# Performance work log

Hardware: AMD Instinct MI355X
Metric: run time of the kernel (lower is better)

The kernel has to match this reference:

```python
import math
import jax, jax.numpy as jnp
import numpy as np

B, T, S = 4, 4096, 1024
HID, CTX, EMB, H = 1024, 768, 1024, 16
D = EMB // H  # head_dim = 64


def setup_inputs() -> dict:
    key = jax.random.key(0)
    ks = jax.random.split(key, 7)
    sc = lambda n: 1.0 / math.sqrt(n)
    return {
        "tokens": jax.random.normal(ks[0], (B, T, HID), jnp.float32),
        "context": jax.random.normal(ks[1], (B, S, CTX), jnp.float32),
        "Wq": jax.random.normal(ks[2], (HID, EMB), jnp.float32) * sc(HID),
        "Wk": jax.random.normal(ks[3], (CTX, EMB), jnp.float32) * sc(CTX),
        "Wv": jax.random.normal(ks[4], (CTX, EMB), jnp.float32) * sc(CTX),
        "Wo": jax.random.normal(ks[5], (EMB, HID), jnp.float32) * sc(EMB),
        "bo": jnp.zeros((HID,), jnp.float32),
    }


def reference(tokens, context, Wq, Wk, Wv, Wo, bo):
    # projections (bias-free, as in torch Linear(bias=False))
    Q = tokens @ Wq              # [B,T,EMB]
    K = context @ Wk             # [B,S,EMB]
    V = context @ Wv             # [B,S,EMB]
    # split heads: B T (H D) -> B H T D
    Q = Q.reshape(B, T, H, D).transpose(0, 2, 1, 3)
    K = K.reshape(B, S, H, D).transpose(0, 2, 1, 3)
    V = V.reshape(B, S, H, D).transpose(0, 2, 1, 3)
    scores = jnp.einsum('bhtd,bhsd->bhts', Q, K) / math.sqrt(D)
    attn = jax.nn.softmax(scores, axis=-1)
    ctx = jnp.einsum('bhts,bhsd->bhtd', attn, V)
    ctx = ctx.transpose(0, 2, 1, 3).reshape(B, T, EMB)
    return ctx @ Wo + bo
```

## Files before the change

kernel.cpp:

```cpp
#include <hip/hip_runtime.h>
#include <hip/hip_bf16.h>

#define B_ 4
#define T_ 4096
#define S_ 1024
#define HID_ 1024
#define CTX_ 768
#define EMB_ 1024
#define H_ 16
#define D_ 64

#define QSCALE 0.18033688011112042f

typedef __attribute__((ext_vector_type(8))) short short8;
typedef __attribute__((ext_vector_type(4))) float f32x4;
typedef __attribute__((ext_vector_type(4))) unsigned short us4;
typedef unsigned short ushort_t;

__device__ inline ushort_t f2b(float f) {
  union { float f; unsigned u; } x; x.f = f;
  return (ushort_t)((x.u + 0x7fffu + ((x.u >> 16) & 1u)) >> 16);
}
__device__ inline unsigned cvtpk2(float a, float b) {
  __hip_bfloat162 h = __float22bfloat162_rn(float2{a, b});
  union { __hip_bfloat162 h; unsigned u; } c; c.h = h; return c.u;
}
__device__ inline ushort_t f2b_fast(float f) {
  __hip_bfloat16 h = __float2bfloat16(f);
  union { __hip_bfloat16 h; ushort_t u; } c; c.h = h; return c.u;
}

using gu32p = const __attribute__((address_space(1))) unsigned int*;
using lu32p = __attribute__((address_space(3))) unsigned int*;
__device__ inline void gload16(const ushort_t* g, ushort_t* l) {
  __builtin_amdgcn_global_load_lds((gu32p)(const void*)g, (lu32p)(void*)l, 16, 0, 0);
}

__device__ inline void conv_body(const float* __restrict__ in, ushort_t* __restrict__ out,
                                 int blk, int tid) {
  const size_t i = ((size_t)blk * 256 + tid) * 8;
  const float4 a = *(const float4*)(in + i);
  const float4 b = *(const float4*)(in + i + 4);
  uint4 u;
  u.x = cvtpk2(a.x, a.y); u.y = cvtpk2(a.z, a.w);
  u.z = cvtpk2(b.x, b.y); u.w = cvtpk2(b.z, b.w);
  *(uint4*)(out + i) = u;
}

__device__ inline void convT_body(const float* __restrict__ W, ushort_t* __restrict__ Wt,
                                  int K, int tile, int tid, float (*Ls)[33]) {
  const int n0 = (tile & 31) * 32, k0 = (tile >> 5) * 32;
  const int r = tid >> 3, c4 = (tid & 7) * 4;
  const float4 v = *(const float4*)&W[(size_t)(k0 + r) * 1024 + n0 + c4];
  Ls[r][c4] = v.x; Ls[r][c4 + 1] = v.y; Ls[r][c4 + 2] = v.z; Ls[r][c4 + 3] = v.w;
  __syncthreads();
  us4 o;
  o.x = f2b_fast(Ls[c4][r]);     o.y = f2b_fast(Ls[c4 + 1][r]);
  o.z = f2b_fast(Ls[c4 + 2][r]); o.w = f2b_fast(Ls[c4 + 3][r]);
  *(us4*)&Wt[(size_t)(n0 + r) * K + k0 + c4] = o;
}

__global__ __launch_bounds__(256) void prepA(
    const float* __restrict__ context,
    const float* __restrict__ Wq, const float* __restrict__ Wk,
    const float* __restrict__ Wv,
    ushort_t* __restrict__ CtxB, ushort_t* __restrict__ WqT,
    ushort_t* __restrict__ WkvT)
{
  __shared__ float Ls[32][33];
  const int tid = threadIdx.x;
  int blk = (int)blockIdx.x;
  if (blk < 1536) { conv_body(context, CtxB, blk, tid); return; }
  blk -= 1536;
  if (blk < 1024) { convT_body(Wq, WqT, 1024, blk, tid, Ls); return; }
  blk -= 1024;
  if (blk < 768)  { convT_body(Wk, WkvT, 768, blk, tid, Ls); return; }
  blk -= 768;
  convT_body(Wv, WkvT + (size_t)1024 * 768, 768, blk, tid, Ls);
}

__global__ __launch_bounds__(256) void prepO(const float* __restrict__ Wo,
                                             ushort_t* __restrict__ WoT) {
  __shared__ float Ls[32][33];
  convT_body(Wo, WoT, 1024, (int)blockIdx.x, threadIdx.x, Ls);
}

__global__ __launch_bounds__(256) void gemm128kv(
    const ushort_t* __restrict__ A, const ushort_t* __restrict__ Bt,
    ushort_t* __restrict__ Kb, ushort_t* __restrict__ Vtb)
{
  __shared__ ushort_t As[128 * 32];
  __shared__ ushort_t Bs[128 * 32];
  const int Kd = CTX_;
  const int tid = threadIdx.x;
  const int bn = blockIdx.x, bm = blockIdx.y;
  const int lane = tid & 63, w = tid >> 6;
  const int lr = lane & 15, lg = lane >> 4;
  const int wr = w >> 1, wc = w & 1;

  f32x4 acc[4][4] = {};

  const int srow = tid >> 2, scol = (tid & 3) * 8;
  const ushort_t* ga = A + (size_t)(bm * 128 + srow) * Kd + scol;
  const ushort_t* gb = Bt + (size_t)(bn * 128 + srow) * Kd + scol;
  ushort_t* la = &As[tid * 8];
  ushort_t* lb = &Bs[tid * 8];
  const size_t rstep = (size_t)64 * Kd;

  for (int k0 = 0; k0 < Kd; k0 += 32) {
    gload16(ga + k0, la);
    gload16(ga + k0 + rstep, la + 2048);
    gload16(gb + k0, lb);
    gload16(gb + k0 + rstep, lb + 2048);
    __syncthreads();
    short8 af[4], bf[4];
#pragma unroll
    for (int m = 0; m < 4; ++m)
      af[m] = *(const short8*)&As[(wr * 64 + m * 16 + lr) * 32 + lg * 8];
#pragma unroll
    for (int n = 0; n < 4; ++n)
      bf[n] = *(const short8*)&Bs[(wc * 64 + n * 16 + lr) * 32 + lg * 8];
#pragma unroll
    for (int m = 0; m < 4; ++m)
#pragma unroll
      for (int n = 0; n < 4; ++n)
        acc[m][n] = __builtin_amdgcn_mfma_f32_16x16x32_bf16(af[m], bf[n], acc[m][n], 0, 0, 0);
    __syncthreads();
  }

  const int row0 = bm * 128 + wr * 64 + lg * 4;
  const int col0 = bn * 128 + wc * 64 + lr;

  if (col0 < 1024) {
#pragma unroll
    for (int m = 0; m < 4; ++m)
#pragma unroll
      for (int n = 0; n < 4; ++n) {
        const int col = col0 + n * 16;
#pragma unroll
        for (int i = 0; i < 4; ++i)
          Kb[(size_t)(row0 + m * 16 + i) * EMB_ + col] = f2b_fast(acc[m][n][i]);
      }
  } else {
#pragma unroll
    for (int m = 0; m < 4; ++m) {
      const int rbase = row0 + m * 16;
      const int bb = rbase >> 10;
      const int s0 = rbase & (S_ - 1);
#pragma unroll
      for (int n = 0; n < 4; ++n) {
        const int vc = col0 + n * 16 - 1024;
        const int hh = vc >> 6, dd = vc & 63;
        us4 o;
        o.x = f2b_fast(acc[m][n][0]); o.y = f2b_fast(acc[m][n][1]);
        o.z = f2b_fast(acc[m][n][2]); o.w = f2b_fast(acc[m][n][3]);
        *(us4*)&Vtb[(((size_t)bb * H_ + hh) * D_ + dd) * S_ + s0] = o;
      }
    }
  }
}

template<int EPI>
__global__ __launch_bounds__(512) void gemm256(
    const ushort_t* __restrict__ A, const ushort_t* __restrict__ Bt,
    void* __restrict__ Cp, const float* __restrict__ bias,
    int M, int Kd, int N)
{
  extern __shared__ ushort_t L[];
  const int tid = threadIdx.x;
  const int lane = tid & 63, wid = tid >> 6;
  const int lr = lane & 15, lg = lane >> 4;
  const int wm = wid >> 2, wn = wid & 3;

  const int cpx = (int)gridDim.x >> 3;
  const int lin = (int)blockIdx.x;
  const int swz = (lin & 7) * cpx + (lin >> 3);
  const int nbn = N >> 8;
  const int bm = swz / nbn, bn = swz % nbn;

  const int sr = tid >> 2;
  const int csrc = (tid & 3) ^ ((sr >> 1) & 3);
  const ushort_t* gA = A + (size_t)(bm * 256 + sr) * Kd + csrc * 8;
  const ushort_t* gB = Bt + (size_t)(bn * 256 + sr) * Kd + csrc * 8;
  const size_t half = (size_t)128 * Kd;
  ushort_t* const dA = L + tid * 8;
  ushort_t* const dB = L + 8192 + tid * 8;

  f32x4 acc[8][4] = {};
  const int NT = Kd >> 5;

#define STAGE256(c) do {                                \
    const int slot_ = ((c) & 3) * 16384;                \
    const int k0_ = (c) << 5;                           \
    gload16(gA + k0_, dA + slot_);                      \
    gload16(gA + k0_ + half, dA + slot_ + 4096);        \
    gload16(gB + k0_, dB + slot_);                      \
    gload16(gB + k0_ + half, dB + slot_ + 4096);        \
  } while (0)

  STAGE256(0); STAGE256(1); STAGE256(2);
  asm volatile("s_waitcnt vmcnt(8)" ::: "memory");
  __builtin_amdgcn_s_barrier();
  __builtin_amdgcn_sched_barrier(0);

  for (int t = 0; t < NT; ++t) {
    if (t + 3 < NT) STAGE256(t + 3);
    const ushort_t* As_ = L + (t & 3) * 16384;
    const ushort_t* Bs_ = As_ + 8192;
    short8 af[8], bf[4];
#pragma unroll
    for (int m = 0; m < 8; ++m) {
      const int row = wm * 128 + m * 16 + lr;
      af[m] = *(const short8*)&As_[row * 32 + (lg ^ ((row >> 1) & 3)) * 8];
    }
#pragma unroll
    for (int n = 0; n < 4; ++n) {
      const int row = wn * 64 + n * 16 + lr;
      bf[n] = *(const short8*)&Bs_[row * 32 + (lg ^ ((row >> 1) & 3)) * 8];
    }
    __builtin_amdgcn_s_setprio(1);
#pragma unroll
    for (int m = 0; m < 8; ++m)
#pragma unroll
      for (int n = 0; n < 4; ++n)
        acc[m][n] = __builtin_amdgcn_mfma_f32_16x16x32_bf16(af[m], bf[n], acc[m][n], 0, 0, 0);
    __builtin_amdgcn_s_setprio(0);
    asm volatile("s_waitcnt vmcnt(8)" ::: "memory");
    __builtin_amdgcn_s_barrier();
    __builtin_amdgcn_sched_barrier(0);
  }
#undef STAGE256

  const int row0 = bm * 256 + wm * 128 + lg * 4;
  const int col0 = bn * 256 + wn * 64 + lr;

  if constexpr (EPI == 3) {
    float* C = (float*)Cp;
#pragma unroll
    for (int n = 0; n < 4; ++n) {
      const int col = col0 + n * 16;
      const float bv = bias[col];
#pragma unroll
      for (int m = 0; m < 8; ++m)
#pragma unroll
        for (int i = 0; i < 4; ++i)
          C[(size_t)(row0 + m * 16 + i) * N + col] = acc[m][n][i] + bv;
    }
  } else {
    ushort_t* C = (ushort_t*)Cp;
#pragma unroll
    for (int m = 0; m < 8; ++m)
#pragma unroll
      for (int n = 0; n < 4; ++n) {
        const int col = col0 + n * 16;
#pragma unroll
        for (int i = 0; i < 4; ++i)
          C[(size_t)(row0 + m * 16 + i) * N + col] = f2b(acc[m][n][i] * QSCALE);
      }
  }
}

__global__ __launch_bounds__(512) void gemm256f(
    const float* __restrict__ Af, const ushort_t* __restrict__ Bt,
    ushort_t* __restrict__ Cp, int M, int N)
{
  constexpr int Kd = 1024, NT = 32;
  extern __shared__ ushort_t L[];
  const int tid = threadIdx.x;
  const int lane = tid & 63, wid = tid >> 6;
  const int lr = lane & 15, lg = lane >> 4;
  const int wm = wid >> 2, wn = wid & 3;

  const int cpx = (int)gridDim.x >> 3;
  const int lin = (int)blockIdx.x;
  const int swz = (lin & 7) * cpx + (lin >> 3);
  const int nbn = N >> 8;
  const int bm = swz / nbn, bn = swz % nbn;

  const int sr = tid >> 2;
  const int csrc = (tid & 3) ^ ((sr >> 1) & 3);
  const float* gA = Af + (size_t)(bm * 256 + sr) * Kd + csrc * 8;
  const ushort_t* gB = Bt + (size_t)(bn * 256 + sr) * Kd + csrc * 8;
  const size_t half = (size_t)128 * Kd;
  ushort_t* const dA = L + tid * 8;
  ushort_t* const dB = L + 8192 + tid * 8;

  f32x4 acc[8][4] = {};
  float4 ra0[4], ra1[4];

#define ALOADF(c, RS) do { const int k0_ = (c) << 5;      \
    RS[0] = *(const float4*)(gA + k0_);                   \
    RS[1] = *(const float4*)(gA + k0_ + 4);               \
    RS[2] = *(const float4*)(gA + k0_ + half);            \
    RS[3] = *(const float4*)(gA + k0_ + half + 4);        \
  } while (0)

#define AWRITE(c, RS) do { const int slot_ = ((c) & 3) * 16384;  \
    uint4 u0, u1;                                                \
    u0.x = cvtpk2(RS[0].x, RS[0].y); u0.y = cvtpk2(RS[0].z, RS[0].w); \
    u0.z = cvtpk2(RS[1].x, RS[1].y); u0.w = cvtpk2(RS[1].z, RS[1].w); \
    u1.x = cvtpk2(RS[2].x, RS[2].y); u1.y = cvtpk2(RS[2].z, RS[2].w); \
    u1.z = cvtpk2(RS[3].x, RS[3].y); u1.w = cvtpk2(RS[3].z, RS[3].w); \
    *(uint4*)(dA + slot_) = u0;                                  \
    *(uint4*)(dA + slot_ + 4096) = u1;                           \
  } while (0)

#define BSTAGE(c) do { const int slot_ = ((c) & 3) * 16384; const int k0_ = (c) << 5; \
    gload16(gB + k0_, dB + slot_);                      \
    gload16(gB + k0_ + half, dB + slot_ + 4096);        \
  } while (0)

#define COMPUTE(c) do {                                                  \
    const ushort_t* As_ = L + ((c) & 3) * 16384;                         \
    const ushort_t* Bs_ = As_ + 8192;                                    \
    short8 af[8], bf[4];                                                 \
    _Pragma("unroll")                                                    \
    for (int m = 0; m < 8; ++m) {                                        \
      const int row = wm * 128 + m * 16 + lr;                            \
      af[m] = *(const short8*)&As_[row * 32 + (lg ^ ((row >> 1) & 3)) * 8]; \
    }                                                                    \
    _Pragma("unroll")                                                    \
    for (int n = 0; n < 4; ++n) {                                        \
      const int row = wn * 64 + n * 16 + lr;                             \
      bf[n] = *(const short8*)&Bs_[row * 32 + (lg ^ ((row >> 1) & 3)) * 8]; \
    }                                                                    \
    __builtin_amdgcn_s_setprio(1);                                       \
    _Pragma("unroll")                                                    \
    for (int m = 0; m < 8; ++m)                                          \
      _Pragma("unroll")                                                  \
      for (int n = 0; n < 4; ++n)                                        \
        acc[m][n] = __builtin_amdgcn_mfma_f32_16x16x32_bf16(af[m], bf[n], acc[m][n], 0, 0, 0); \
    __builtin_amdgcn_s_setprio(0);                                       \
  } while (0)

#define ENDBAR do {                                        \
    asm volatile("s_waitcnt lgkmcnt(0)" ::: "memory");     \
    __builtin_amdgcn_s_barrier();                          \
    __builtin_amdgcn_sched_barrier(0);                     \
  } while (0)

  {
    float4 p0[4], p1[4], p2[4];
    ALOADF(0, p0); ALOADF(1, p1); ALOADF(2, p2);
    AWRITE(0, p0); AWRITE(1, p1); AWRITE(2, p2);
    BSTAGE(0); BSTAGE(1); BSTAGE(2);
    ALOADF(3, ra1);
    asm volatile("s_waitcnt vmcnt(4)" ::: "memory");
    ENDBAR;
  }

  for (int t = 0; t < NT; t += 2) {
    if (t + 3 < NT) { AWRITE(t + 3, ra1); BSTAGE(t + 3); }
    if (t + 4 < NT) ALOADF(t + 4, ra0);
    COMPUTE(t);
    ENDBAR;
    if (t + 4 < NT) { AWRITE(t + 4, ra0); BSTAGE(t + 4); }
    if (t + 5 < NT) ALOADF(t + 5, ra1);
    COMPUTE(t + 1);
    ENDBAR;
  }
#undef ALOADF
#undef AWRITE
#undef BSTAGE
#undef COMPUTE
#undef ENDBAR

  const int row0 = bm * 256 + wm * 128 + lg * 4;
  const int col0 = bn * 256 + wn * 64 + lr;
#pragma unroll
  for (int m = 0; m < 8; ++m)
#pragma unroll
    for (int n = 0; n < 4; ++n) {
      const int col = col0 + n * 16;
#pragma unroll
      for (int i = 0; i < 4; ++i)
        Cp[(size_t)(row0 + m * 16 + i) * N + col] = f2b(acc[m][n][i] * QSCALE);
    }
}

__global__ __launch_bounds__(512) void attn_v5r(
    const ushort_t* __restrict__ Q, const ushort_t* __restrict__ K,
    const ushort_t* __restrict__ Vt, ushort_t* __restrict__ C)
{
  __shared__ ushort_t Ks[2][64 * 64];
  __shared__ ushort_t Vs[2][64 * 64];
  __shared__ ushort_t Ps[8][16][72];
  const int tid = threadIdx.x;
  const int lane = tid & 63, w = tid >> 6;
  const int lr = lane & 15, lg = lane >> 4;

  const int bid = (int)blockIdx.x;
  const int g = (bid & 7) | (((bid >> 3) >> 4) << 3);
  const int tb = (bid >> 3) & 15;
  const int h = g & 15, b = g >> 4;
  const int t0 = tb * 256;

  short8 qf[2][2];
#pragma unroll
  for (int qs = 0; qs < 2; ++qs) {
    const size_t qrow = (size_t)b * T_ + t0 + w * 32 + qs * 16 + lr;
    const ushort_t* qp = Q + qrow * EMB_ + h * 64;
    qf[qs][0] = *(const short8*)(qp + lg * 8);
    qf[qs][1] = *(const short8*)(qp + 32 + lg * 8);
  }

  short8 ones;
#pragma unroll
  for (int j = 0; j < 8; ++j) ones[j] = (short)0x3F80;

  f32x4 o[2][4] = {};
  f32x4 lacc[2] = {};

  const int srow = tid >> 3, schunk = tid & 7;
  const int sswz = schunk ^ (srow & 7);
  const ushort_t* kg = K + ((size_t)b * S_ + srow) * EMB_ + h * 64 + sswz * 8;
  const ushort_t* vg = Vt + (((size_t)b * H_ + h) * D_ + srow) * S_ + sswz * 8;

  gload16(kg, &Ks[0][tid * 8]);
  gload16(vg, &Vs[0][tid * 8]);

  int cur = 0;
  for (int st = 0; st < S_ / 64; ++st) {
    __syncthreads();
    if (st + 1 < S_ / 64) {
      gload16(kg + (size_t)(st + 1) * 64 * EMB_, &Ks[cur ^ 1][tid * 8]);
      gload16(vg + (st + 1) * 64, &Vs[cur ^ 1][tid * 8]);
    }

    f32x4 sacc[2][4] = {};
    __builtin_amdgcn_s_setprio(1);
#pragma unroll
    for (int c = 0; c < 4; ++c) {
      const int krow = c * 16 + lr;
      const int sw = krow & 7;
      const short8 ka0 = *(const short8*)&Ks[cur][krow * 64 + ((lg ^ sw) * 8)];
      const short8 ka1 = *(const short8*)&Ks[cur][krow * 64 + (((4 + lg) ^ sw) * 8)];
#pragma unroll
      for (int qs = 0; qs < 2; ++qs) {
        sacc[qs][c] = __builtin_amdgcn_mfma_f32_16x16x32_bf16(ka0, qf[qs][0], sacc[qs][c], 0, 0, 0);
        sacc[qs][c] = __builtin_amdgcn_mfma_f32_16x16x32_bf16(ka1, qf[qs][1], sacc[qs][c], 0, 0, 0);
      }
    }
    __builtin_amdgcn_s_setprio(0);

    short8 pa[2][2];
#pragma unroll
    for (int qs = 0; qs < 2; ++qs) {
#pragma unroll
      for (int c = 0; c < 4; ++c) {
        uint2 pk;
        pk.x = cvtpk2(exp2f(sacc[qs][c][0]), exp2f(sacc[qs][c][1]));
        pk.y = cvtpk2(exp2f(sacc[qs][c][2]), exp2f(sacc[qs][c][3]));
        *(uint2*)&Ps[w][lr][c * 16 + lg * 4] = pk;
      }
      pa[qs][0] = *(const short8*)&Ps[w][lr][lg * 8];
      pa[qs][1] = *(const short8*)&Ps[w][lr][32 + lg * 8];
    }

    __builtin_amdgcn_s_setprio(1);
#pragma unroll
    for (int sh = 0; sh < 2; ++sh) {
#pragma unroll
      for (int dc = 0; dc < 4; ++dc) {
        const int vrow = dc * 16 + lr;
        const int vsw = vrow & 7;
        const short8 vb = *(const short8*)&Vs[cur][vrow * 64 + (((sh * 4 + lg) ^ vsw) * 8)];
        o[0][dc] = __builtin_amdgcn_mfma_f32_16x16x32_bf16(pa[0][sh], vb, o[0][dc], 0, 0, 0);
        o[1][dc] = __builtin_amdgcn_mfma_f32_16x16x32_bf16(pa[1][sh], vb, o[1][dc], 0, 0, 0);
      }
      lacc[0] = __builtin_amdgcn_mfma_f32_16x16x32_bf16(pa[0][sh], ones, lacc[0], 0, 0, 0);
      lacc[1] = __builtin_amdgcn_mfma_f32_16x16x32_bf16(pa[1][sh], ones, lacc[1], 0, 0, 0);
    }
    __builtin_amdgcn_s_setprio(0);

    cur ^= 1;
  }

#pragma unroll
  for (int qs = 0; qs < 2; ++qs) {
#pragma unroll
    for (int i = 0; i < 4; ++i) {
      const float li = 1.0f / lacc[qs][i];
      const size_t trow = (size_t)b * T_ + t0 + w * 32 + qs * 16 + lg * 4 + i;
#pragma unroll
      for (int dc = 0; dc < 4; ++dc)
        C[trow * EMB_ + h * 64 + dc * 16 + lr] = f2b_fast(o[qs][dc][i] * li);
    }
  }
}

extern "C" void kernel_launch(void* const* d_in, const int* in_sizes, int n_in,
                              void* d_out, int out_size, void* d_ws, size_t ws_size,
                              hipStream_t stream) {
  const float* tokens  = (const float*)d_in[0];
  const float* context = (const float*)d_in[1];
  const float* Wq = (const float*)d_in[2];
  const float* Wk = (const float*)d_in[3];
  const float* Wv = (const float*)d_in[4];
  const float* Wo = (const float*)d_in[5];
  const float* bo = (const float*)d_in[6];
  float* out = (float*)d_out;

  ushort_t* Qb  = (ushort_t*)d_out;
  ushort_t* Kb   = (ushort_t*)d_ws;
  ushort_t* Vtb  = Kb + (size_t)B_ * S_ * EMB_;
  ushort_t* Cb   = Vtb + (size_t)B_ * S_ * EMB_;
  ushort_t* WqT  = Cb + (size_t)B_ * T_ * EMB_;
  ushort_t* WkvT = WqT + (size_t)EMB_ * HID_;

  prepA<<<4096, 256, 0, stream>>>(context, Wq, Wk, Wv, Cb, WqT, WkvT);
  gemm256f<<<dim3((B_ * T_ / 256) * (EMB_ / 256)), 512, 131072, stream>>>(
      tokens, WqT, Qb, B_ * T_, EMB_);
  prepO<<<1024, 256, 0, stream>>>(Wo, WqT);
  gemm128kv<<<dim3(16, 32), 256, 0, stream>>>(Cb, WkvT, Kb, Vtb);
  attn_v5r<<<dim3((T_ / 256) * H_ * B_), 512, 0, stream>>>(Qb, Kb, Vtb, Cb);
  gemm256<3><<<dim3((B_ * T_ / 256) * (HID_ / 256)), 512, 131072, stream>>>(
      Cb, WqT, out, bo, B_ * T_, EMB_, HID_);
}
```

Before: 231.2 us.

## Triple-buffer K/V projection GEMM and attention loads with vmcnt waits

The K/V projection GEMM moves from a 128x128 tile with 256 threads and synchronous single-buffered loads to a 128x256 tile with 512 threads. It adds a swizzled LDS layout, a block-index remap and a three-stage async pipeline that uses explicit vmcnt waits and a single barrier per step. The attention kernel's K/V staging goes from double to triple buffering in dynamic shared memory, issuing loads two tiles ahead. The aim is to hide global load latency and cut barrier stalls, at the cost of more LDS per block and possibly lower occupancy.

After: 226.9 us. No clear change (-1.9%).

```diff
diff --git a/kernel.cpp b/kernel.cpp
--- a/kernel.cpp
+++ b/kernel.cpp
@@ -85,51 +85,71 @@
   convT_body(Wo, WoT, 1024, (int)blockIdx.x, threadIdx.x, Ls);
 }
 
-__global__ __launch_bounds__(256) void gemm128kv(
+__global__ __launch_bounds__(512) void gemm256kv(
     const ushort_t* __restrict__ A, const ushort_t* __restrict__ Bt,
     ushort_t* __restrict__ Kb, ushort_t* __restrict__ Vtb)
 {
-  __shared__ ushort_t As[128 * 32];
-  __shared__ ushort_t Bs[128 * 32];
-  const int Kd = CTX_;
+  constexpr int Kd = CTX_, NT = CTX_ / 32;
+  extern __shared__ ushort_t L[];
   const int tid = threadIdx.x;
-  const int bn = blockIdx.x, bm = blockIdx.y;
-  const int lane = tid & 63, w = tid >> 6;
+  const int lane = tid & 63, wid = tid >> 6;
   const int lr = lane & 15, lg = lane >> 4;
-  const int wr = w >> 1, wc = w & 1;
+  const int wm = wid >> 2, wn = wid & 3;
+
+  const int lin = (int)blockIdx.x;
+  const int swz = (lin & 7) * 32 + (lin >> 3);
+  const int bm = swz >> 3, bn = swz & 7;
+
+  const int sr = tid >> 2;
+  const int csrc = (tid & 3) ^ ((sr >> 1) & 3);
+  const ushort_t* gA = A + (size_t)(bm * 128 + sr) * Kd + csrc * 8;
+  const ushort_t* gB = Bt + (size_t)(bn * 256 + sr) * Kd + csrc * 8;
+  const size_t halfB = (size_t)128 * Kd;
 
   f32x4 acc[4][4] = {};
 
-  const int srow = tid >> 2, scol = (tid & 3) * 8;
-  const ushort_t* ga = A + (size_t)(bm * 128 + srow) * Kd + scol;
-  const ushort_t* gb = Bt + (size_t)(bn * 128 + srow) * Kd + scol;
-  ushort_t* la = &As[tid * 8];
-  ushort_t* lb = &Bs[tid * 8];
-  const size_t rstep = (size_t)64 * Kd;
-
-  for (int k0 = 0; k0 < Kd; k0 += 32) {
-    gload16(ga + k0, la);
-    gload16(ga + k0 + rstep, la + 2048);
-    gload16(gb + k0, lb);
-    gload16(gb + k0 + rstep, lb + 2048);
-    __syncthreads();
+#define KVSTAGE(c, slot) do { const int k0_ = (c) << 5;            \
+    ushort_t* s_ = L + (slot) * 12288;                             \
+    gload16(gA + k0_, s_ + tid * 8);                               \
+    gload16(gB + k0_, s_ + 4096 + tid * 8);                        \
+    gload16(gB + k0_ + halfB, s_ + 8192 + tid * 8);                \
+  } while (0)
+
+  KVSTAGE(0, 0); KVSTAGE(1, 1);
+  int cur = 0, sls = 2;
+  for (int t = 0; t < NT; ++t) {
+    if (t < NT - 1) asm volatile("s_waitcnt vmcnt(3)" ::: "memory");
+    else            asm volatile("s_waitcnt vmcnt(0)" ::: "memory");
+    __builtin_amdgcn_s_barrier();
+    __builtin_amdgcn_sched_barrier(0);
+    if (t + 2 < NT) KVSTAGE(t + 2, sls);
+    const ushort_t* As_ = L + cur * 12288;
+    const ushort_t* Bs_ = As_ + 4096;
     short8 af[4], bf[4];
 #pragma unroll
-    for (int m = 0; m < 4; ++m)
-      af[m] = *(const short8*)&As[(wr * 64 + m * 16 + lr) * 32 + lg * 8];
-#pragma unroll
-    for (int n = 0; n < 4; ++n)
-      bf[n] = *(const short8*)&Bs[(wc * 64 + n * 16 + lr) * 32 + lg * 8];
+    for (int m = 0; m < 4; ++m) {
+      const int row = wm * 64 + m * 16 + lr;
+      af[m] = *(const short8*)&As_[row * 32 + (lg ^ ((row >> 1) & 3)) * 8];
+    }
+#pragma unroll
+    for (int n = 0; n < 4; ++n) {
+      const int row = wn * 64 + n * 16 + lr;
+      bf[n] = *(const short8*)&Bs_[row * 32 + (lg ^ ((row >> 1) & 3)) * 8];
+    }
+    __builtin_amdgcn_s_setprio(1);
 #pragma unroll
     for (int m = 0; m < 4; ++m)
 #pragma unroll
       for (int n = 0; n < 4; ++n)
         acc[m][n] = __builtin_amdgcn_mfma_f32_16x16x32_bf16(af[m], bf[n], acc[m][n], 0, 0, 0);
-    __syncthreads();
-  }
-
-  const int row0 = bm * 128 + wr * 64 + lg * 4;
-  const int col0 = bn * 128 + wc * 64 + lr;
+    __builtin_amdgcn_s_setprio(0);
+    cur = (cur == 2) ? 0 : cur + 1;
+    sls = (sls == 2) ? 0 : sls + 1;
+  }
+#undef KVSTAGE
+
+  const int row0 = bm * 128 + wm * 64 + lg * 4;
+  const int col0 = bn * 256 + wn * 64 + lr;
 
   if (col0 < 1024) {
 #pragma unroll
@@ -378,13 +398,11 @@
     }
 }
 
-__global__ __launch_bounds__(512) void attn_v5r(
+__global__ __launch_bounds__(512) void attn_v8(
     const ushort_t* __restrict__ Q, const ushort_t* __restrict__ K,
     const ushort_t* __restrict__ Vt, ushort_t* __restrict__ C)
 {
-  __shared__ ushort_t Ks[2][64 * 64];
-  __shared__ ushort_t Vs[2][64 * 64];
-  __shared__ ushort_t Ps[8][16][72];
+  extern __shared__ ushort_t SM[];
   const int tid = threadIdx.x;
   const int lane = tid & 63, w = tid >> 6;
   const int lr = lane & 15, lg = lane >> 4;
@@ -415,17 +433,25 @@
   const int sswz = schunk ^ (srow & 7);
   const ushort_t* kg = K + ((size_t)b * S_ + srow) * EMB_ + h * 64 + sswz * 8;
   const ushort_t* vg = Vt + (((size_t)b * H_ + h) * D_ + srow) * S_ + sswz * 8;
-
-  gload16(kg, &Ks[0][tid * 8]);
-  gload16(vg, &Vs[0][tid * 8]);
-
-  int cur = 0;
-  for (int st = 0; st < S_ / 64; ++st) {
-    __syncthreads();
-    if (st + 1 < S_ / 64) {
-      gload16(kg + (size_t)(st + 1) * 64 * EMB_, &Ks[cur ^ 1][tid * 8]);
-      gload16(vg + (st + 1) * 64, &Vs[cur ^ 1][tid * 8]);
-    }
+  ushort_t* Psw = SM + 24576 + w * 1152;
+
+  gload16(kg, SM + tid * 8);
+  gload16(vg, SM + 12288 + tid * 8);
+  gload16(kg + (size_t)64 * EMB_, SM + 4096 + tid * 8);
+  gload16(vg + 64, SM + 12288 + 4096 + tid * 8);
+
+  int cur = 0, sls = 2;
+  for (int st = 0; st < 16; ++st) {
+    if (st < 15) asm volatile("s_waitcnt vmcnt(2)" ::: "memory");
+    else         asm volatile("s_waitcnt vmcnt(0)" ::: "memory");
+    __builtin_amdgcn_s_barrier();
+    __builtin_amdgcn_sched_barrier(0);
+    if (st + 2 < 16) {
+      gload16(kg + (size_t)(st + 2) * 64 * EMB_, SM + sls * 4096 + tid * 8);
+      gload16(vg + (st + 2) * 64, SM + 12288 + sls * 4096 + tid * 8);
+    }
+    const ushort_t* Ksb = SM + cur * 4096;
+    const ushort_t* Vsb = SM + 12288 + cur * 4096;
 
     f32x4 sacc[2][4] = {};
     __builtin_amdgcn_s_setprio(1);
@@ -433,8 +459,8 @@
     for (int c = 0; c < 4; ++c) {
       const int krow = c * 16 + lr;
       const int sw = krow & 7;
-      const short8 ka0 = *(const short8*)&Ks[cur][krow * 64 + ((lg ^ sw) * 8)];
-      const short8 ka1 = *(const short8*)&Ks[cur][krow * 64 + (((4 + lg) ^ sw) * 8)];
+      const short8 ka0 = *(const short8*)&Ksb[krow * 64 + ((lg ^ sw) * 8)];
+      const short8 ka1 = *(const short8*)&Ksb[krow * 64 + (((4 + lg) ^ sw) * 8)];
 #pragma unroll
       for (int qs = 0; qs < 2; ++qs) {
         sacc[qs][c] = __builtin_amdgcn_mfma_f32_16x16x32_bf16(ka0, qf[qs][0], sacc[qs][c], 0, 0, 0);
@@ -451,10 +477,10 @@
         uint2 pk;
         pk.x = cvtpk2(exp2f(sacc[qs][c][0]), exp2f(sacc[qs][c][1]));
         pk.y = cvtpk2(exp2f(sacc[qs][c][2]), exp2f(sacc[qs][c][3]));
-        *(uint2*)&Ps[w][lr][c * 16 + lg * 4] = pk;
+        *(uint2*)&Psw[lr * 72 + c * 16 + lg * 4] = pk;
       }
-      pa[qs][0] = *(const short8*)&Ps[w][lr][lg * 8];
-      pa[qs][1] = *(const short8*)&Ps[w][lr][32 + lg * 8];
+      pa[qs][0] = *(const short8*)&Psw[lr * 72 + lg * 8];
+      pa[qs][1] = *(const short8*)&Psw[lr * 72 + 32 + lg * 8];
     }
 
     __builtin_amdgcn_s_setprio(1);
@@ -464,7 +490,7 @@
       for (int dc = 0; dc < 4; ++dc) {
         const int vrow = dc * 16 + lr;
         const int vsw = vrow & 7;
-        const short8 vb = *(const short8*)&Vs[cur][vrow * 64 + (((sh * 4 + lg) ^ vsw) * 8)];
+        const short8 vb = *(const short8*)&Vsb[vrow * 64 + (((sh * 4 + lg) ^ vsw) * 8)];
         o[0][dc] = __builtin_amdgcn_mfma_f32_16x16x32_bf16(pa[0][sh], vb, o[0][dc], 0, 0, 0);
         o[1][dc] = __builtin_amdgcn_mfma_f32_16x16x32_bf16(pa[1][sh], vb, o[1][dc], 0, 0, 0);
       }
@@ -473,7 +499,8 @@
     }
     __builtin_amdgcn_s_setprio(0);
 
-    cur ^= 1;
+    cur = (cur == 2) ? 0 : cur + 1;
+    sls = (sls == 2) ? 0 : sls + 1;
   }
 
 #pragma unroll
@@ -512,8 +539,8 @@
   gemm256f<<<dim3((B_ * T_ / 256) * (EMB_ / 256)), 512, 131072, stream>>>(
       tokens, WqT, Qb, B_ * T_, EMB_);
   prepO<<<1024, 256, 0, stream>>>(Wo, WqT);
-  gemm128kv<<<dim3(16, 32), 256, 0, stream>>>(Cb, WkvT, Kb, Vtb);
-  attn_v5r<<<dim3((T_ / 256) * H_ * B_), 512, 0, stream>>>(Qb, Kb, Vtb, Cb);
+  gemm256kv<<<dim3(256), 512, 73728, stream>>>(Cb, WkvT, Kb, Vtb);
+  attn_v8<<<dim3((T_ / 256) * H_ * B_), 512, 67584, stream>>>(Qb, Kb, Vtb, Cb);
   gemm256<3><<<dim3((B_ * T_ / 256) * (HID_ / 256)), 512, 131072, stream>>>(
       Cb, WqT, out, bo, B_ * T_, EMB_, HID_);
 }
```
